# Optimization experiments

Hardware: AMD Instinct MI355X
Metric: run time of the kernel (lower is better)

The kernel has to match this reference:

```python
import jax, jax.numpy as jnp
import numpy as np

N = 100000   # nodes
E = 640000   # edges
D = 128      # init_node == hidden_node
L = 3        # layers (len('gcn_gcn_gcn'.split('_')))


def setup_inputs() -> dict:
    key = jax.random.key(0)
    ks = jax.random.split(key, 17)
    p = lambda k, shape: jax.random.normal(k, shape, jnp.float32) * 0.05
    return {
        "x": jax.random.normal(ks[0], (N, D), jnp.float32),
        "edge_attr": jax.random.uniform(ks[1], (E,), jnp.float32),
        "edge_index": jax.random.randint(ks[2], (2, E), 0, N),
        "conv_w": p(ks[3], (L, D, D)),       # SparseConv.weight
        "conv_lin_w": p(ks[4], (L, D, D)),   # SparseConv.lin (no bias)
        "l1_w": p(ks[5], (L, D, D)), "l1_b": p(ks[6], (L, D)),
        "l2_w": p(ks[7], (L, D, D)), "l2_b": p(ks[8], (L, D)),
        "mlp1_w": p(ks[9], (L, 2 * D, D)), "mlp1_b": p(ks[10], (L, D)),
        "mlp2_w": p(ks[11], (L, D, D)), "mlp2_b": p(ks[12], (L, D)),
        "post1_w": p(ks[13], (D, D)), "post1_b": p(ks[14], (D,)),
        "post2_w": p(ks[15], (D, D)), "post2_b": p(ks[16], (D,)),
    }


def reference(x, edge_attr, edge_index, conv_w, conv_lin_w,
              l1_w, l1_b, l2_w, l2_b, mlp1_w, mlp1_b, mlp2_w, mlp2_b,
              post1_w, post1_b, post2_w, post2_b):
    src, dst = edge_index[0], edge_index[1]  # PyG: message h_j from src, scatter-add at dst
    n = x.shape[0]

    def agg(h):
        # gather source features, weight per edge, scatter-add at targets
        return jax.ops.segment_sum(edge_attr[:, None] * h[src], dst, num_segments=n)

    mask = None
    for i in range(L):
        # --- WeightConv: computes sigmoid gate ---
        xm = x if mask is None else x * mask
        h = xm @ l1_w[i] + l1_b[i]
        w = jnp.concatenate([agg(h), xm @ l2_w[i] + l2_b[i]], axis=-1)  # [N, 2D]
        w = jax.nn.relu(jax.nn.relu(w) @ mlp1_w[i] + mlp1_b[i])
        mask = jax.nn.sigmoid(w @ mlp2_w[i] + mlp2_b[i])  # [N, D]
        # --- SparseConv: masked transform + propagate + residual lin ---
        h2 = (x * mask) @ conv_w[i]
        x = jax.nn.relu((agg(h2) + x @ conv_lin_w[i]) * mask)
    x = jax.nn.relu(x @ post1_w + post1_b)
    # F.dropout omitted (deterministic reference)
    return x @ post2_w + post2_b
```

## Files before the change

### kernel.cpp

```cpp
#include <hip/hip_runtime.h>
#include <math.h>

#define NN 100000
#define EE 640000
#define DD 128
#define NB_SCAN ((NN + 255) / 256)

typedef __attribute__((ext_vector_type(8))) short bf16x8;
typedef __attribute__((ext_vector_type(4))) float f32x4;

static __device__ __forceinline__ float4 ld4(const float* p) {
    return *reinterpret_cast<const float4*>(p);
}

static __device__ __forceinline__ unsigned short f2bf(float x) {
    unsigned u = __float_as_uint(x);
    return (unsigned short)((u + 0x7FFFu + ((u >> 16) & 1u)) >> 16);
}

static __device__ __forceinline__ void splitbf(float a, short& hi, short& lo) {
    unsigned u = __float_as_uint(a);
    unsigned hr = (u + 0x7FFFu + ((u >> 16) & 1u)) >> 16;
    float hf = __uint_as_float(hr << 16);
    float l = a - hf;
    unsigned ul = __float_as_uint(l);
    unsigned lr = (ul + 0x7FFFu + ((ul >> 16) & 1u)) >> 16;
    hi = (short)hr; lo = (short)lr;
}

__global__ void wfrag_k(const float* __restrict__ l1w, const float* __restrict__ l2w,
                        const float* __restrict__ mlp1w, const float* __restrict__ mlp2w,
                        const float* __restrict__ convw, const float* __restrict__ convlinw,
                        const float* __restrict__ post1w, const float* __restrict__ post2w,
                        unsigned short* __restrict__ Wh, unsigned short* __restrict__ Wl)
{
    const int b = blockIdx.x;
    const float* W; int slice; size_t fbase; int K;
    if (b < 12)      { W = l1w;      slice = b;      fbase = 0;      K = 128; }
    else if (b < 24) { W = l2w;      slice = b - 12; fbase = 49152;  K = 128; }
    else if (b < 48) { W = mlp1w;    slice = b - 24; fbase = 98304;  K = 256; }
    else if (b < 60) { W = mlp2w;    slice = b - 48; fbase = 196608; K = 128; }
    else if (b < 72) { W = convw;    slice = b - 60; fbase = 245760; K = 128; }
    else if (b < 84) { W = convlinw; slice = b - 72; fbase = 294912; K = 128; }
    else if (b < 88) { W = post1w;   slice = b - 84; fbase = 344064; K = 128; }
    else             { W = post2w;   slice = b - 88; fbase = 360448; K = 128; }
    const int kslices = K / 32;
    const int mat = slice / kslices;
    const int ks  = slice % kslices;
    const float* Wm = W + (size_t)mat * K * DD;
    const size_t outb = fbase + (size_t)mat * K * DD + (size_t)ks * 4096;
    const int t = threadIdx.x;
#pragma unroll
    for (int e = 0; e < 16; ++e) {
        const int f = t * 16 + e;
        const int r = f & 7, lane = (f >> 3) & 63, ct = f >> 9;
        const int krow = ks * 32 + (lane >> 4) * 8 + r;
        const int col  = ct * 16 + (lane & 15);
        short hh, ll;
        splitbf(Wm[(size_t)krow * DD + col], hh, ll);
        Wh[outb + f] = (unsigned short)hh; Wl[outb + f] = (unsigned short)ll;
    }
}

template<int KT, int DUAL, int RAW1, int MINW>
__launch_bounds__(256, MINW)
__global__ void gemm_f32A(const float* __restrict__ A,
                          const float* __restrict__ Amask,
                          const unsigned short* __restrict__ Wh0,
                          const unsigned short* __restrict__ Wl0,
                          const float* __restrict__ bias0, const int act0, const int obf0,
                          void* __restrict__ out0, const int ldo0, const int co0,
                          const unsigned short* __restrict__ Wh1,
                          const unsigned short* __restrict__ Wl1,
                          const float* __restrict__ bias1, const int obf1,
                          void* __restrict__ out1, const int ldo1, const int co1)
{
    __shared__ __align__(16) unsigned short Bs[16384];
    const int t = threadIdx.x, lane = t & 63, w = t >> 6;
    const int kg = lane >> 4, c16 = lane & 15;
    const int rb = blockIdx.x * 64 + w * 16;
    int ra = rb + c16; if (ra >= NN) ra = NN - 1;

    bf16x8 ah[KT], al[KT];
    bf16x8 uh[RAW1 ? KT : 1], ul[RAW1 ? KT : 1];
#pragma unroll
    for (int ks = 0; ks < KT; ++ks) {
        const float* ap = A + (size_t)ra * (KT * 32) + ks * 32 + kg * 8;
        const float4 v0 = ld4(ap), v1 = ld4(ap + 4);
        float tmp[8] = {v0.x, v0.y, v0.z, v0.w, v1.x, v1.y, v1.z, v1.w};
        if (RAW1) {
#pragma unroll
            for (int j = 0; j < 8; ++j) { short hh, ll; splitbf(tmp[j], hh, ll); uh[ks][j] = hh; ul[ks][j] = ll; }
        }
        if (Amask) {
            const float* mp = Amask + (size_t)ra * DD + ks * 32 + kg * 8;
            const float4 m0 = ld4(mp), m1 = ld4(mp + 4);
            tmp[0] *= m0.x; tmp[1] *= m0.y; tmp[2] *= m0.z; tmp[3] *= m0.w;
            tmp[4] *= m1.x; tmp[5] *= m1.y; tmp[6] *= m1.z; tmp[7] *= m1.w;
        }
#pragma unroll
        for (int j = 0; j < 8; ++j) { short hh, ll; splitbf(tmp[j], hh, ll); ah[ks][j] = hh; al[ks][j] = ll; }
    }

    auto pass = [&](const unsigned short* Wh, const unsigned short* Wl,
                    const bf16x8* xh, const bf16x8* xl,
                    const float* bias, const int act, const int obf,
                    void* out, const int ldo, const int co, const bool first) {
        f32x4 acc[8];
#pragma unroll
        for (int ct = 0; ct < 8; ++ct) acc[ct] = f32x4{0.f, 0.f, 0.f, 0.f};
#pragma unroll
        for (int st = 0; st < KT / 2; ++st) {
            if (!(first && st == 0)) __syncthreads();
#pragma unroll
            for (int i = 0; i < 4; ++i) {
                const int idx = i * 2048 + t * 8;
                *(uint4*)&Bs[idx]        = *(const uint4*)&Wh[(size_t)st * 8192 + idx];
                *(uint4*)&Bs[8192 + idx] = *(const uint4*)&Wl[(size_t)st * 8192 + idx];
            }
            __syncthreads();
#pragma unroll
            for (int s = 0; s < 2; ++s) {
                const int ks = st * 2 + s;
#pragma unroll
                for (int ct = 0; ct < 8; ++ct) {
                    const int fo = ((s * 8 + ct) * 64 + lane) * 8;
                    const bf16x8 bh = *(const bf16x8*)&Bs[fo];
                    const bf16x8 bl = *(const bf16x8*)&Bs[8192 + fo];
                    acc[ct] = __builtin_amdgcn_mfma_f32_16x16x32_bf16(xh[ks], bh, acc[ct], 0, 0, 0);
                    acc[ct] = __builtin_amdgcn_mfma_f32_16x16x32_bf16(xl[ks], bh, acc[ct], 0, 0, 0);
                    acc[ct] = __builtin_amdgcn_mfma_f32_16x16x32_bf16(xh[ks], bl, acc[ct], 0, 0, 0);
                }
            }
        }
#pragma unroll
        for (int ct = 0; ct < 8; ++ct) {
            const int c = ct * 16 + c16;
            const float b = bias ? bias[c] : 0.f;
#pragma unroll
            for (int r = 0; r < 4; ++r) {
                const int row = rb + kg * 4 + r;
                if (row < NN) {
                    float v = acc[ct][r] + b;
                    if (act == 1) v = fmaxf(v, 0.f);
                    if (obf) ((unsigned short*)out)[(size_t)row * ldo + co + c] = f2bf(v);
                    else     ((float*)out)[(size_t)row * ldo + co + c] = v;
                }
            }
        }
    };

    pass(Wh0, Wl0, ah, al, bias0, act0, obf0, out0, ldo0, co0, true);
    if (DUAL)
        pass(Wh1, Wl1, RAW1 ? uh : ah, RAW1 ? ul : al, bias1, 0, obf1, out1, ldo1, co1, false);
}

template<int KT, int MINW>
__launch_bounds__(256, MINW)
__global__ void gemm_bf16A(const unsigned short* __restrict__ A, const int reluA,
                           const unsigned short* __restrict__ Wh,
                           const unsigned short* __restrict__ Wl,
                           const float* __restrict__ bias, const int act, const int obf,
                           void* __restrict__ out, const int ldo, const int co)
{
    __shared__ __align__(16) unsigned short Bs[16384];
    const int t = threadIdx.x, lane = t & 63, w = t >> 6;
    const int kg = lane >> 4, c16 = lane & 15;
    const int rb = blockIdx.x * 64 + w * 16;
    int ra = rb + c16; if (ra >= NN) ra = NN - 1;

    bf16x8 ah[KT];
#pragma unroll
    for (int ks = 0; ks < KT; ++ks) {
        bf16x8 av = *(const bf16x8*)(A + (size_t)ra * (KT * 32) + ks * 32 + kg * 8);
        if (reluA) {
#pragma unroll
            for (int j = 0; j < 8; ++j) av[j] = (av[j] < 0) ? (short)0 : av[j];
        }
        ah[ks] = av;
    }

    f32x4 acc[8];
#pragma unroll
    for (int ct = 0; ct < 8; ++ct) acc[ct] = f32x4{0.f, 0.f, 0.f, 0.f};
#pragma unroll
    for (int st = 0; st < KT / 2; ++st) {
        if (st) __syncthreads();
#pragma unroll
        for (int i = 0; i < 4; ++i) {
            const int idx = i * 2048 + t * 8;
            *(uint4*)&Bs[idx]        = *(const uint4*)&Wh[(size_t)st * 8192 + idx];
            *(uint4*)&Bs[8192 + idx] = *(const uint4*)&Wl[(size_t)st * 8192 + idx];
        }
        __syncthreads();
#pragma unroll
        for (int s = 0; s < 2; ++s) {
            const int ks = st * 2 + s;
#pragma unroll
            for (int ct = 0; ct < 8; ++ct) {
                const int fo = ((s * 8 + ct) * 64 + lane) * 8;
                const bf16x8 bh = *(const bf16x8*)&Bs[fo];
                const bf16x8 bl = *(const bf16x8*)&Bs[8192 + fo];
                acc[ct] = __builtin_amdgcn_mfma_f32_16x16x32_bf16(ah[ks], bh, acc[ct], 0, 0, 0);
                acc[ct] = __builtin_amdgcn_mfma_f32_16x16x32_bf16(ah[ks], bl, acc[ct], 0, 0, 0);
            }
        }
    }
#pragma unroll
    for (int ct = 0; ct < 8; ++ct) {
        const int c = ct * 16 + c16;
        const float b = bias ? bias[c] : 0.f;
#pragma unroll
        for (int r = 0; r < 4; ++r) {
            const int row = rb + kg * 4 + r;
            if (row < NN) {
                float v = acc[ct][r] + b;
                if (act == 1) v = fmaxf(v, 0.f);
                else if (act == 2) v = 1.f / (1.f + __expf(-v));
                if (obf) ((unsigned short*)out)[(size_t)row * ldo + co + c] = f2bf(v);
                else     ((float*)out)[(size_t)row * ldo + co + c] = v;
            }
        }
    }
}

__launch_bounds__(256)
__global__ void spmm_bf16(const unsigned int* __restrict__ H2,
                          const int* __restrict__ rp,
                          const int* __restrict__ ccol,
                          const float* __restrict__ cval,
                          const float* __restrict__ addend,
                          const float* __restrict__ pmask,
                          const int act, const int obf,
                          float* __restrict__ outf, unsigned int* __restrict__ outb,
                          const int ldo)
{
    const int w = (blockIdx.x * 256 + threadIdx.x) >> 6;
    if (w >= NN) return;
    const int lane = threadIdx.x & 63;
    const int s = rp[w], e = rp[w + 1];
    float ax = 0.f, ay = 0.f;
    int j = s;
    while (j < e) {
        int cnt = e - j; if (cnt > 8) cnt = 8;
        int cols[8]; float vals[8];
#pragma unroll
        for (int q = 0; q < 8; ++q) {
            if (q < cnt) { cols[q] = ccol[j + q]; vals[q] = cval[j + q]; }
        }
#pragma unroll
        for (int q = 0; q < 8; ++q) {
            if (q < cnt) {
                const unsigned u = H2[(size_t)cols[q] * 64 + lane];
                ax = fmaf(vals[q], __uint_as_float(u << 16), ax);
                ay = fmaf(vals[q], __uint_as_float(u & 0xFFFF0000u), ay);
            }
        }
        j += cnt;
    }
    if (addend) {
        const float2 t = *reinterpret_cast<const float2*>(addend + (size_t)w * DD + lane * 2);
        ax += t.x; ay += t.y;
    }
    if (pmask) {
        const float2 m = *reinterpret_cast<const float2*>(pmask + (size_t)w * DD + lane * 2);
        ax *= m.x; ay *= m.y;
    }
    if (act == 1) { ax = fmaxf(ax, 0.f); ay = fmaxf(ay, 0.f); }
    if (obf) {
        outb[(size_t)w * ldo + lane] = (unsigned)f2bf(ax) | ((unsigned)f2bf(ay) << 16);
    } else {
        float2 o; o.x = ax; o.y = ay;
        *reinterpret_cast<float2*>(outf + (size_t)w * ldo + lane * 2) = o;
    }
}

__global__ void hist_k(const int* __restrict__ dstI, int* __restrict__ counts) {
    const int e = blockIdx.x * 256 + threadIdx.x;
    if (e < EE) atomicAdd(&counts[dstI[e]], 1);
}

__global__ void block_sums_k(const int* __restrict__ counts, int* __restrict__ bsum) {
    __shared__ int s[256];
    const int t = threadIdx.x;
    const int i = blockIdx.x * 256 + t;
    s[t] = (i < NN) ? counts[i] : 0;
    __syncthreads();
    for (int off = 128; off > 0; off >>= 1) {
        if (t < off) s[t] += s[t + off];
        __syncthreads();
    }
    if (t == 0) bsum[blockIdx.x] = s[0];
}

__global__ void scan_bsums_k(const int* __restrict__ bsum, int* __restrict__ bpre, const int nb) {
    __shared__ int s[512];
    const int t = threadIdx.x;
    s[t] = (t < nb) ? bsum[t] : 0;
    __syncthreads();
    for (int off = 1; off < 512; off <<= 1) {
        const int tmp = (t >= off) ? s[t - off] : 0;
        __syncthreads();
        s[t] += tmp;
        __syncthreads();
    }
    if (t < nb) bpre[t] = (t == 0) ? 0 : s[t - 1];
}

__global__ void scan_final_k(const int* __restrict__ counts, const int* __restrict__ bpre,
                             int* __restrict__ rowptr, int* __restrict__ nextc) {
    __shared__ int s[256];
    const int t = threadIdx.x;
    const int i = blockIdx.x * 256 + t;
    const int v = (i < NN) ? counts[i] : 0;
    s[t] = v;
    __syncthreads();
    for (int off = 1; off < 256; off <<= 1) {
        const int tmp = (t >= off) ? s[t - off] : 0;
        __syncthreads();
        s[t] += tmp;
        __syncthreads();
    }
    const int excl = s[t] - v + bpre[blockIdx.x];
    if (i < NN) { rowptr[i] = excl; nextc[i] = excl; }
    if (i == NN - 1) rowptr[NN] = EE;
}

__global__ void scatter_k(const int* __restrict__ srcI, const int* __restrict__ dstI,
                          const float* __restrict__ ea, int* __restrict__ nextc,
                          int* __restrict__ ccol, float* __restrict__ cval) {
    const int e = blockIdx.x * 256 + threadIdx.x;
    if (e >= EE) return;
    const int d = dstI[e];
    const int p = atomicAdd(&nextc[d], 1);
    ccol[p] = srcI[e];
    cval[p] = ea[e];
}

extern "C" void kernel_launch(void* const* d_in, const int* in_sizes, int n_in,
                              void* d_out, int out_size, void* d_ws, size_t ws_size,
                              hipStream_t stream)
{
    const float* x_in0      = (const float*)d_in[0];
    const float* edge_attr  = (const float*)d_in[1];
    const int*   edge_index = (const int*)d_in[2];
    const float* l1_b       = (const float*)d_in[6];
    const float* l2_b       = (const float*)d_in[8];
    const float* mlp1_b     = (const float*)d_in[10];
    const float* mlp2_b     = (const float*)d_in[12];
    const float* post1_b    = (const float*)d_in[14];
    const float* post2_b    = (const float*)d_in[16];

    const int* srcI = edge_index;
    const int* dstI = edge_index + EE;

    float* x_ws = (float*)d_out;

    float*          maskb  = (float*)d_ws;
    float*          tbuf   = maskb + (size_t)NN * DD;
    unsigned short* h16    = (unsigned short*)(tbuf + (size_t)NN * DD);
    unsigned short* cat16  = h16 + (size_t)NN * DD;
    unsigned short* gh16   = cat16 + (size_t)NN * 2 * DD;
    unsigned short* Wh_all = gh16 + (size_t)NN * DD;
    unsigned short* Wl_all = Wh_all + 376832;
    float* cval   = (float*)(Wl_all + 376832);
    int*   ccol   = (int*)(cval + EE);
    int*   rowptr = ccol + EE;
    int*   nextc  = rowptr + (NN + 1);
    int*   counts = nextc + NN;
    int*   bsum   = counts + NN;
    int*   bpre   = bsum + 512;

    wfrag_k<<<92, 256, 0, stream>>>((const float*)d_in[5], (const float*)d_in[7],
                                    (const float*)d_in[9], (const float*)d_in[11],
                                    (const float*)d_in[3], (const float*)d_in[4],
                                    (const float*)d_in[13], (const float*)d_in[15],
                                    Wh_all, Wl_all);
    hipMemsetAsync(counts, 0, NN * sizeof(int), stream);
    hist_k      <<<(EE + 255) / 256, 256, 0, stream>>>(dstI, counts);
    block_sums_k<<<NB_SCAN, 256, 0, stream>>>(counts, bsum);
    scan_bsums_k<<<1, 512, 0, stream>>>(bsum, bpre, NB_SCAN);
    scan_final_k<<<NB_SCAN, 256, 0, stream>>>(counts, bpre, rowptr, nextc);
    scatter_k   <<<(EE + 255) / 256, 256, 0, stream>>>(srcI, dstI, edge_attr, nextc, ccol, cval);

    const int GG = (NN + 63) / 64;
    const int SPMM_GRID = NN * 64 / 256;

    const size_t F_L1 = 0, F_L2 = 49152, F_M1 = 98304, F_M2 = 196608;
    const size_t F_CV = 245760, F_CL = 294912, F_P1 = 344064, F_P2 = 360448;

    for (int i = 0; i < 3; ++i) {
        const float* xc = (i == 0) ? x_in0 : x_ws;
        const float* pm = (i == 0) ? nullptr : maskb;
        const size_t o128 = (size_t)i * 16384, o256 = (size_t)i * 32768;
        gemm_f32A<4, 1, 0, 4><<<GG, 256, 0, stream>>>(xc, pm,
            Wh_all + F_L1 + o128, Wl_all + F_L1 + o128, l1_b + (size_t)i * DD, 0, 1, h16, DD, 0,
            Wh_all + F_L2 + o128, Wl_all + F_L2 + o128, l2_b + (size_t)i * DD, 1, cat16, 2 * DD, DD);
        spmm_bf16<<<SPMM_GRID, 256, 0, stream>>>((const unsigned*)h16, rowptr, ccol, cval,
            nullptr, nullptr, 0, 1, nullptr, (unsigned*)cat16, 2 * DD / 2);
        gemm_bf16A<8, 4><<<GG, 256, 0, stream>>>(cat16, 1,
            Wh_all + F_M1 + o256, Wl_all + F_M1 + o256, mlp1_b + (size_t)i * DD, 1, 1, gh16, DD, 0);
        gemm_bf16A<4, 4><<<GG, 256, 0, stream>>>(gh16, 0,
            Wh_all + F_M2 + o128, Wl_all + F_M2 + o128, mlp2_b + (size_t)i * DD, 2, 0, maskb, DD, 0);
        gemm_f32A<4, 1, 1, 3><<<GG, 256, 0, stream>>>(xc, maskb,
            Wh_all + F_CV + o128, Wl_all + F_CV + o128, nullptr, 0, 1, h16, DD, 0,
            Wh_all + F_CL + o128, Wl_all + F_CL + o128, nullptr, 0, tbuf, DD, 0);
        spmm_bf16<<<SPMM_GRID, 256, 0, stream>>>((const unsigned*)h16, rowptr, ccol, cval,
            tbuf, maskb, 1, 0, x_ws, nullptr, DD);
    }
    gemm_f32A<4, 0, 0, 4><<<GG, 256, 0, stream>>>(x_ws, nullptr,
        Wh_all + F_P1, Wl_all + F_P1, post1_b, 1, 1, gh16, DD, 0,
        nullptr, nullptr, nullptr, 0, nullptr, 0, 0);
    gemm_bf16A<4, 4><<<GG, 256, 0, stream>>>(gh16, 0,
        Wh_all + F_P2, Wl_all + F_P2, post2_b, 0, 0, (float*)d_out, DD, 0);

    (void)in_sizes; (void)n_in; (void)out_size; (void)ws_size;
}
```

Before: 1.187 ms.

## Fuse MLP GEMM pairs, store x as bf16 hi/lo splits, vectorize epilogues

```diff
diff --git a/kernel.cpp b/kernel.cpp
--- a/kernel.cpp
+++ b/kernel.cpp
@@ -5,34 +5,46 @@
 #define EE 640000
 #define DD 128
 #define NB_SCAN ((NN + 255) / 256)
+#define GG 1563
 
 typedef __attribute__((ext_vector_type(8))) short bf16x8;
 typedef __attribute__((ext_vector_type(4))) float f32x4;
+typedef unsigned short ush;
+typedef unsigned int uint;
 
 static __device__ __forceinline__ float4 ld4(const float* p) {
     return *reinterpret_cast<const float4*>(p);
 }
-
-static __device__ __forceinline__ unsigned short f2bf(float x) {
+static __device__ __forceinline__ ush f2bf(float x) {
     unsigned u = __float_as_uint(x);
-    return (unsigned short)((u + 0x7FFFu + ((u >> 16) & 1u)) >> 16);
-}
-
+    return (ush)((u + 0x7FFFu + ((u >> 16) & 1u)) >> 16);
+}
+static __device__ __forceinline__ float bf2f(short h) {
+    return __uint_as_float(((unsigned)(ush)h) << 16);
+}
 static __device__ __forceinline__ void splitbf(float a, short& hi, short& lo) {
     unsigned u = __float_as_uint(a);
     unsigned hr = (u + 0x7FFFu + ((u >> 16) & 1u)) >> 16;
-    float hf = __uint_as_float(hr << 16);
-    float l = a - hf;
+    float l = a - __uint_as_float(hr << 16);
     unsigned ul = __float_as_uint(l);
-    unsigned lr = (ul + 0x7FFFu + ((ul >> 16) & 1u)) >> 16;
-    hi = (short)hr; lo = (short)lr;
+    hi = (short)hr; lo = (short)((ul + 0x7FFFu + ((ul >> 16) & 1u)) >> 16);
+}
+static __device__ __forceinline__ void splitbf_t(float a, short& hi, short& lo) {
+    unsigned u = __float_as_uint(a);
+    hi = (short)(u >> 16);
+    float l = a - __uint_as_float(u & 0xFFFF0000u);
+    lo = (short)(__float_as_uint(l) >> 16);
+}
+
+static __device__ __forceinline__ f32x4 MFMA(bf16x8 a, bf16x8 b, f32x4 c) {
+    return __builtin_amdgcn_mfma_f32_16x16x32_bf16(a, b, c, 0, 0, 0);
 }
 
 __global__ void wfrag_k(const float* __restrict__ l1w, const float* __restrict__ l2w,
                         const float* __restrict__ mlp1w, const float* __restrict__ mlp2w,
                         const float* __restrict__ convw, const float* __restrict__ convlinw,
                         const float* __restrict__ post1w, const float* __restrict__ post2w,
-                        unsigned short* __restrict__ Wh, unsigned short* __restrict__ Wl)
+                        ush* __restrict__ Wh, ush* __restrict__ Wl)
 {
     const int b = blockIdx.x;
     const float* W; int slice; size_t fbase; int K;
@@ -55,142 +67,238 @@
         const int f = t * 16 + e;
         const int r = f & 7, lane = (f >> 3) & 63, ct = f >> 9;
         const int krow = ks * 32 + (lane >> 4) * 8 + r;
-        const int col  = ct * 16 + (lane & 15);
+        const int col  = (lane & 15) * 8 + ct;
         short hh, ll;
         splitbf(Wm[(size_t)krow * DD + col], hh, ll);
-        Wh[outb + f] = (unsigned short)hh; Wl[outb + f] = (unsigned short)ll;
-    }
-}
-
-template<int KT, int DUAL, int RAW1, int MINW>
+        Wh[outb + f] = (ush)hh; Wl[outb + f] = (ush)ll;
+    }
+}
+
+template<bool THREE>
+static __device__ __forceinline__ void mfma_pass128(
+    const bf16x8* xh, const bf16x8* xl,
+    const ush* __restrict__ Wh, const ush* __restrict__ Wl,
+    ush* Bs, const int t, const int lane, const bool first, f32x4* acc)
+{
+#pragma unroll
+    for (int ct = 0; ct < 8; ++ct) acc[ct] = f32x4{0.f, 0.f, 0.f, 0.f};
+#pragma unroll
+    for (int st = 0; st < 2; ++st) {
+        if (!(first && st == 0)) __syncthreads();
+#pragma unroll
+        for (int i = 0; i < 4; ++i) {
+            const int idx = i * 2048 + t * 8;
+            *(uint4*)&Bs[idx]        = *(const uint4*)&Wh[(size_t)st * 8192 + idx];
+            *(uint4*)&Bs[8192 + idx] = *(const uint4*)&Wl[(size_t)st * 8192 + idx];
+        }
+        __syncthreads();
+#pragma unroll
+        for (int s = 0; s < 2; ++s) {
+            const int ks = st * 2 + s;
+#pragma unroll
+            for (int ct = 0; ct < 8; ++ct) {
+                const int fo = ((s * 8 + ct) * 64 + lane) * 8;
+                const bf16x8 bh = *(const bf16x8*)&Bs[fo];
+                const bf16x8 bl = *(const bf16x8*)&Bs[8192 + fo];
+                acc[ct] = MFMA(xh[ks], bh, acc[ct]);
+                if (THREE) acc[ct] = MFMA(xl[ks], bh, acc[ct]);
+                acc[ct] = MFMA(xh[ks], bl, acc[ct]);
+            }
+        }
+    }
+}
+
+static __device__ __forceinline__ void epi_store(
+    const f32x4* acc, const float* __restrict__ bias, const int act, const int obf,
+    void* __restrict__ out, const int ldo, const int co,
+    const int rb, const int kg, const int c16)
+{
+    float bv[8];
+    if (bias) {
+        const float4 b0 = ld4(bias + c16 * 8), b1 = ld4(bias + c16 * 8 + 4);
+        bv[0]=b0.x; bv[1]=b0.y; bv[2]=b0.z; bv[3]=b0.w;
+        bv[4]=b1.x; bv[5]=b1.y; bv[6]=b1.z; bv[7]=b1.w;
+    } else {
+#pragma unroll
+        for (int j = 0; j < 8; ++j) bv[j] = 0.f;
+    }
+#pragma unroll
+    for (int r = 0; r < 4; ++r) {
+        const int row = rb + kg * 4 + r;
+        if (row < NN) {
+            float v[8];
+#pragma unroll
+            for (int ct = 0; ct < 8; ++ct) {
+                v[ct] = acc[ct][r] + bv[ct];
+                if (act == 1) v[ct] = fmaxf(v[ct], 0.f);
+                else if (act == 2) v[ct] = 1.f / (1.f + __expf(-v[ct]));
+            }
+            if (obf) {
+                uint4 pk;
+                pk.x = (uint)f2bf(v[0]) | ((uint)f2bf(v[1]) << 16);
+                pk.y = (uint)f2bf(v[2]) | ((uint)f2bf(v[3]) << 16);
+                pk.z = (uint)f2bf(v[4]) | ((uint)f2bf(v[5]) << 16);
+                pk.w = (uint)f2bf(v[6]) | ((uint)f2bf(v[7]) << 16);
+                *(uint4*)((ush*)out + (size_t)row * ldo + co + c16 * 8) = pk;
+            } else {
+                float* op = (float*)out + (size_t)row * ldo + co + c16 * 8;
+                *(float4*)op       = make_float4(v[0], v[1], v[2], v[3]);
+                *(float4*)(op + 4) = make_float4(v[4], v[5], v[6], v[7]);
+            }
+        }
+    }
+}
+
+template<int RAW1, int MINW>
 __launch_bounds__(256, MINW)
 __global__ void gemm_f32A(const float* __restrict__ A,
                           const float* __restrict__ Amask,
-                          const unsigned short* __restrict__ Wh0,
-                          const unsigned short* __restrict__ Wl0,
+                          const ush* __restrict__ Wh0, const ush* __restrict__ Wl0,
                           const float* __restrict__ bias0, const int act0, const int obf0,
                           void* __restrict__ out0, const int ldo0, const int co0,
-                          const unsigned short* __restrict__ Wh1,
-                          const unsigned short* __restrict__ Wl1,
-                          const float* __restrict__ bias1, const int obf1,
+                          const ush* __restrict__ Wh1, const ush* __restrict__ Wl1,
+                          const float* __restrict__ bias1, const int act1, const int obf1,
                           void* __restrict__ out1, const int ldo1, const int co1)
 {
-    __shared__ __align__(16) unsigned short Bs[16384];
+    __shared__ __align__(16) ush Bs[16384];
     const int t = threadIdx.x, lane = t & 63, w = t >> 6;
     const int kg = lane >> 4, c16 = lane & 15;
     const int rb = blockIdx.x * 64 + w * 16;
     int ra = rb + c16; if (ra >= NN) ra = NN - 1;
 
-    bf16x8 ah[KT], al[KT];
-    bf16x8 uh[RAW1 ? KT : 1], ul[RAW1 ? KT : 1];
-#pragma unroll
-    for (int ks = 0; ks < KT; ++ks) {
-        const float* ap = A + (size_t)ra * (KT * 32) + ks * 32 + kg * 8;
+    bf16x8 ah[4], al[4];
+    bf16x8 uh[RAW1 ? 4 : 1], ul[RAW1 ? 4 : 1];
+#pragma unroll
+    for (int ks = 0; ks < 4; ++ks) {
+        const float* ap = A + (size_t)ra * DD + ks * 32 + kg * 8;
         const float4 v0 = ld4(ap), v1 = ld4(ap + 4);
         float tmp[8] = {v0.x, v0.y, v0.z, v0.w, v1.x, v1.y, v1.z, v1.w};
         if (RAW1) {
 #pragma unroll
-            for (int j = 0; j < 8; ++j) { short hh, ll; splitbf(tmp[j], hh, ll); uh[ks][j] = hh; ul[ks][j] = ll; }
+            for (int j = 0; j < 8; ++j) { short hh, ll; splitbf_t(tmp[j], hh, ll); uh[ks][j] = hh; ul[ks][j] = ll; }
         }
         if (Amask) {
             const float* mp = Amask + (size_t)ra * DD + ks * 32 + kg * 8;
             const float4 m0 = ld4(mp), m1 = ld4(mp + 4);
-            tmp[0] *= m0.x; tmp[1] *= m0.y; tmp[2] *= m0.z; tmp[3] *= m0.w;
-            tmp[4] *= m1.x; tmp[5] *= m1.y; tmp[6] *= m1.z; tmp[7] *= m1.w;
-        }
-#pragma unroll
-        for (int j = 0; j < 8; ++j) { short hh, ll; splitbf(tmp[j], hh, ll); ah[ks][j] = hh; al[ks][j] = ll; }
-    }
-
-    auto pass = [&](const unsigned short* Wh, const unsigned short* Wl,
-                    const bf16x8* xh, const bf16x8* xl,
-                    const float* bias, const int act, const int obf,
-                    void* out, const int ldo, const int co, const bool first) {
-        f32x4 acc[8];
-#pragma unroll
-        for (int ct = 0; ct < 8; ++ct) acc[ct] = f32x4{0.f, 0.f, 0.f, 0.f};
-#pragma unroll
-        for (int st = 0; st < KT / 2; ++st) {
-            if (!(first && st == 0)) __syncthreads();
-#pragma unroll
-            for (int i = 0; i < 4; ++i) {
-                const int idx = i * 2048 + t * 8;
-                *(uint4*)&Bs[idx]        = *(const uint4*)&Wh[(size_t)st * 8192 + idx];
-                *(uint4*)&Bs[8192 + idx] = *(const uint4*)&Wl[(size_t)st * 8192 + idx];
-            }
-            __syncthreads();
-#pragma unroll
-            for (int s = 0; s < 2; ++s) {
-                const int ks = st * 2 + s;
-#pragma unroll
-                for (int ct = 0; ct < 8; ++ct) {
-                    const int fo = ((s * 8 + ct) * 64 + lane) * 8;
-                    const bf16x8 bh = *(const bf16x8*)&Bs[fo];
-                    const bf16x8 bl = *(const bf16x8*)&Bs[8192 + fo];
-                    acc[ct] = __builtin_amdgcn_mfma_f32_16x16x32_bf16(xh[ks], bh, acc[ct], 0, 0, 0);
-                    acc[ct] = __builtin_amdgcn_mfma_f32_16x16x32_bf16(xl[ks], bh, acc[ct], 0, 0, 0);
-                    acc[ct] = __builtin_amdgcn_mfma_f32_16x16x32_bf16(xh[ks], bl, acc[ct], 0, 0, 0);
-                }
-            }
-        }
-#pragma unroll
-        for (int ct = 0; ct < 8; ++ct) {
-            const int c = ct * 16 + c16;
-            const float b = bias ? bias[c] : 0.f;
-#pragma unroll
-            for (int r = 0; r < 4; ++r) {
-                const int row = rb + kg * 4 + r;
-                if (row < NN) {
-                    float v = acc[ct][r] + b;
-                    if (act == 1) v = fmaxf(v, 0.f);
-                    if (obf) ((unsigned short*)out)[(size_t)row * ldo + co + c] = f2bf(v);
-                    else     ((float*)out)[(size_t)row * ldo + co + c] = v;
-                }
-            }
-        }
-    };
-
-    pass(Wh0, Wl0, ah, al, bias0, act0, obf0, out0, ldo0, co0, true);
-    if (DUAL)
-        pass(Wh1, Wl1, RAW1 ? uh : ah, RAW1 ? ul : al, bias1, 0, obf1, out1, ldo1, co1, false);
-}
-
-template<int KT, int MINW>
-__launch_bounds__(256, MINW)
-__global__ void gemm_bf16A(const unsigned short* __restrict__ A, const int reluA,
-                           const unsigned short* __restrict__ Wh,
-                           const unsigned short* __restrict__ Wl,
-                           const float* __restrict__ bias, const int act, const int obf,
-                           void* __restrict__ out, const int ldo, const int co)
-{
-    __shared__ __align__(16) unsigned short Bs[16384];
+            tmp[0]*=m0.x; tmp[1]*=m0.y; tmp[2]*=m0.z; tmp[3]*=m0.w;
+            tmp[4]*=m1.x; tmp[5]*=m1.y; tmp[6]*=m1.z; tmp[7]*=m1.w;
+        }
+#pragma unroll
+        for (int j = 0; j < 8; ++j) { short hh, ll; splitbf_t(tmp[j], hh, ll); ah[ks][j] = hh; al[ks][j] = ll; }
+    }
+
+    f32x4 acc[8];
+    mfma_pass128<true>(ah, al, Wh0, Wl0, Bs, t, lane, true, acc);
+    epi_store(acc, bias0, act0, obf0, out0, ldo0, co0, rb, kg, c16);
+    mfma_pass128<true>(RAW1 ? uh : ah, RAW1 ? ul : al, Wh1, Wl1, Bs, t, lane, false, acc);
+    epi_store(acc, bias1, act1, obf1, out1, ldo1, co1, rb, kg, c16);
+}
+
+__launch_bounds__(256, 4)
+__global__ void gemm_xm(const ush* __restrict__ Ah, const ush* __restrict__ Al,
+                        const ush* __restrict__ Wh0, const ush* __restrict__ Wl0,
+                        const float* __restrict__ bias0, void* __restrict__ out0,
+                        const int ldo0, const int co0,
+                        const ush* __restrict__ Wh1, const ush* __restrict__ Wl1,
+                        const float* __restrict__ bias1, void* __restrict__ out1,
+                        const int ldo1, const int co1)
+{
+    __shared__ __align__(16) ush Bs[16384];
     const int t = threadIdx.x, lane = t & 63, w = t >> 6;
     const int kg = lane >> 4, c16 = lane & 15;
     const int rb = blockIdx.x * 64 + w * 16;
     int ra = rb + c16; if (ra >= NN) ra = NN - 1;
 
-    bf16x8 ah[KT];
-#pragma unroll
-    for (int ks = 0; ks < KT; ++ks) {
-        bf16x8 av = *(const bf16x8*)(A + (size_t)ra * (KT * 32) + ks * 32 + kg * 8);
+    bf16x8 amh[4], aml[4];
+#pragma unroll
+    for (int ks = 0; ks < 4; ++ks) {
+        amh[ks] = *(const bf16x8*)(Ah + (size_t)ra * DD + ks * 32 + kg * 8);
+        aml[ks] = *(const bf16x8*)(Al + (size_t)ra * DD + ks * 32 + kg * 8);
+    }
+    f32x4 acc[8];
+    mfma_pass128<true>(amh, aml, Wh0, Wl0, Bs, t, lane, true, acc);
+    epi_store(acc, bias0, 0, 1, out0, ldo0, co0, rb, kg, c16);
+    mfma_pass128<true>(amh, aml, Wh1, Wl1, Bs, t, lane, false, acc);
+    epi_store(acc, bias1, 0, 1, out1, ldo1, co1, rb, kg, c16);
+}
+
+__launch_bounds__(256, 3)
+__global__ void gemm_conv(const ush* __restrict__ Ah, const ush* __restrict__ Al,
+                          const float* __restrict__ mask,
+                          const ush* __restrict__ WhC, const ush* __restrict__ WlC,
+                          void* __restrict__ outH,
+                          const ush* __restrict__ WhL, const ush* __restrict__ WlL,
+                          void* __restrict__ outT)
+{
+    __shared__ __align__(16) ush Bs[16384];
+    const int t = threadIdx.x, lane = t & 63, w = t >> 6;
+    const int kg = lane >> 4, c16 = lane & 15;
+    const int rb = blockIdx.x * 64 + w * 16;
+    int ra = rb + c16; if (ra >= NN) ra = NN - 1;
+
+    bf16x8 uh[4], ul[4], amh[4], aml[4];
+#pragma unroll
+    for (int ks = 0; ks < 4; ++ks) {
+        uh[ks] = *(const bf16x8*)(Ah + (size_t)ra * DD + ks * 32 + kg * 8);
+        ul[ks] = *(const bf16x8*)(Al + (size_t)ra * DD + ks * 32 + kg * 8);
+        const float* mp = mask + (size_t)ra * DD + ks * 32 + kg * 8;
+        const float4 m0 = ld4(mp), m1 = ld4(mp + 4);
+        const float mv[8] = {m0.x, m0.y, m0.z, m0.w, m1.x, m1.y, m1.z, m1.w};
+#pragma unroll
+        for (int j = 0; j < 8; ++j) {
+            const float af = bf2f(uh[ks][j]) + bf2f(ul[ks][j]);
+            short hh, ll; splitbf_t(af * mv[j], hh, ll);
+            amh[ks][j] = hh; aml[ks][j] = ll;
+        }
+    }
+    f32x4 acc[8];
+    mfma_pass128<true>(amh, aml, WhC, WlC, Bs, t, lane, true, acc);
+    epi_store(acc, nullptr, 0, 1, outH, DD, 0, rb, kg, c16);
+    mfma_pass128<true>(uh, ul, WhL, WlL, Bs, t, lane, false, acc);
+    epi_store(acc, nullptr, 0, 1, outT, DD, 0, rb, kg, c16);
+}
+
+template<int KT1, int AHL, int SIGE>
+__launch_bounds__(256, 3)
+__global__ void gemm_fused2(const ush* __restrict__ Aa, const ush* __restrict__ Ab,
+                            const int reluA,
+                            const ush* __restrict__ W1h, const ush* __restrict__ W1l,
+                            const float* __restrict__ b1,
+                            const ush* __restrict__ W2h, const ush* __restrict__ W2l,
+                            const float* __restrict__ b2,
+                            float* __restrict__ out)
+{
+    __shared__ __align__(16) ush Bs[16384];
+    __shared__ __align__(16) ush Ts[8192];
+    const int t = threadIdx.x, lane = t & 63, w = t >> 6;
+    const int kg = lane >> 4, c16 = lane & 15;
+    const int rb = blockIdx.x * 64 + w * 16;
+    int ra = rb + c16; if (ra >= NN) ra = NN - 1;
+    char* tsb = (char*)&Ts[w * 2048];
+
+    bf16x8 a1h[KT1], a1l[AHL ? KT1 : 1];
+#pragma unroll
+    for (int ks = 0; ks < KT1; ++ks) {
+        bf16x8 av = *(const bf16x8*)(Aa + (size_t)ra * (KT1 * 32) + ks * 32 + kg * 8);
         if (reluA) {
 #pragma unroll
             for (int j = 0; j < 8; ++j) av[j] = (av[j] < 0) ? (short)0 : av[j];
         }
-        ah[ks] = av;
+        a1h[ks] = av;
+        if (AHL) a1l[ks] = *(const bf16x8*)(Ab + (size_t)ra * (KT1 * 32) + ks * 32 + kg * 8);
     }
 
     f32x4 acc[8];
 #pragma unroll
     for (int ct = 0; ct < 8; ++ct) acc[ct] = f32x4{0.f, 0.f, 0.f, 0.f};
 #pragma unroll
-    for (int st = 0; st < KT / 2; ++st) {
+    for (int st = 0; st < KT1 / 2; ++st) {
         if (st) __syncthreads();
 #pragma unroll
         for (int i = 0; i < 4; ++i) {
             const int idx = i * 2048 + t * 8;
-            *(uint4*)&Bs[idx]        = *(const uint4*)&Wh[(size_t)st * 8192 + idx];
-            *(uint4*)&Bs[8192 + idx] = *(const uint4*)&Wl[(size_t)st * 8192 + idx];
+            *(uint4*)&Bs[idx]        = *(const uint4*)&W1h[(size_t)st * 8192 + idx];
+            *(uint4*)&Bs[8192 + idx] = *(const uint4*)&W1l[(size_t)st * 8192 + idx];
         }
         __syncthreads();
 #pragma unroll
@@ -201,39 +309,73 @@
                 const int fo = ((s * 8 + ct) * 64 + lane) * 8;
                 const bf16x8 bh = *(const bf16x8*)&Bs[fo];
                 const bf16x8 bl = *(const bf16x8*)&Bs[8192 + fo];
-                acc[ct] = __builtin_amdgcn_mfma_f32_16x16x32_bf16(ah[ks], bh, acc[ct], 0, 0, 0);
-                acc[ct] = __builtin_amdgcn_mfma_f32_16x16x32_bf16(ah[ks], bl, acc[ct], 0, 0, 0);
+                acc[ct] = MFMA(a1h[ks], bh, acc[ct]);
+                if (AHL) acc[ct] = MFMA(a1l[ks], bh, acc[ct]);
+                acc[ct] = MFMA(a1h[ks], bl, acc[ct]);
             }
         }
     }
-#pragma unroll
-    for (int ct = 0; ct < 8; ++ct) {
-        const int c = ct * 16 + c16;
-        const float b = bias ? bias[c] : 0.f;
+
+    {
+        const float4 b0 = ld4(b1 + c16 * 8), b1v = ld4(b1 + c16 * 8 + 4);
+        const float bv[8] = {b0.x, b0.y, b0.z, b0.w, b1v.x, b1v.y, b1v.z, b1v.w};
 #pragma unroll
         for (int r = 0; r < 4; ++r) {
-            const int row = rb + kg * 4 + r;
-            if (row < NN) {
-                float v = acc[ct][r] + b;
-                if (act == 1) v = fmaxf(v, 0.f);
-                else if (act == 2) v = 1.f / (1.f + __expf(-v));
-                if (obf) ((unsigned short*)out)[(size_t)row * ldo + co + c] = f2bf(v);
-                else     ((float*)out)[(size_t)row * ldo + co + c] = v;
+            const int row = kg * 4 + r;
+            bf16x8 pk;
+#pragma unroll
+            for (int ct = 0; ct < 8; ++ct)
+                pk[ct] = (short)f2bf(fmaxf(acc[ct][r] + bv[ct], 0.f));
+            const int byte = (row * 256 + c16 * 16) ^ ((row & 7) << 4);
+            *(bf16x8*)(tsb + byte) = pk;
+        }
+    }
+    bf16x8 a2[4];
+#pragma unroll
+    for (int ks2 = 0; ks2 < 4; ++ks2) {
+        const int byte = (c16 * 256 + ks2 * 64 + kg * 16) ^ ((c16 & 7) << 4);
+        a2[ks2] = *(const bf16x8*)(tsb + byte);
+    }
+
+#pragma unroll
+    for (int ct = 0; ct < 8; ++ct) acc[ct] = f32x4{0.f, 0.f, 0.f, 0.f};
+#pragma unroll
+    for (int st = 0; st < 2; ++st) {
+        __syncthreads();
+#pragma unroll
+        for (int i = 0; i < 4; ++i) {
+            const int idx = i * 2048 + t * 8;
+            *(uint4*)&Bs[idx]        = *(const uint4*)&W2h[(size_t)st * 8192 + idx];
+            *(uint4*)&Bs[8192 + idx] = *(const uint4*)&W2l[(size_t)st * 8192 + idx];
+        }
+        __syncthreads();
+#pragma unroll
+        for (int s = 0; s < 2; ++s) {
+            const int ks = st * 2 + s;
+#pragma unroll
+            for (int ct = 0; ct < 8; ++ct) {
+                const int fo = ((s * 8 + ct) * 64 + lane) * 8;
+                const bf16x8 bh = *(const bf16x8*)&Bs[fo];
+                const bf16x8 bl = *(const bf16x8*)&Bs[8192 + fo];
+                acc[ct] = MFMA(a2[ks], bh, acc[ct]);
+                acc[ct] = MFMA(a2[ks], bl, acc[ct]);
             }
         }
     }
-}
-
+    epi_store(acc, b2, SIGE ? 2 : 0, 0, out, DD, 0, rb, kg, c16);
+}
+
+template<int XOUT>
 __launch_bounds__(256)
-__global__ void spmm_bf16(const unsigned int* __restrict__ H2,
-                          const int* __restrict__ rp,
-                          const int* __restrict__ ccol,
-                          const float* __restrict__ cval,
-                          const float* __restrict__ addend,
-                          const float* __restrict__ pmask,
-                          const int act, const int obf,
-                          float* __restrict__ outf, unsigned int* __restrict__ outb,
-                          const int ldo)
+__global__ void spmm_b(const uint* __restrict__ H2,
+                       const int* __restrict__ rp,
+                       const int* __restrict__ ccol,
+                       const float* __restrict__ cval,
+                       const uint* __restrict__ tadd,
+                       const float* __restrict__ pmask,
+                       uint* __restrict__ o0, uint* __restrict__ o1,
+                       uint* __restrict__ o2, uint* __restrict__ o3,
+                       const int ldo, const int writeXM)
 {
     const int w = (blockIdx.x * 256 + threadIdx.x) >> 6;
     if (w >= NN) return;
@@ -245,33 +387,38 @@
         int cnt = e - j; if (cnt > 8) cnt = 8;
         int cols[8]; float vals[8];
 #pragma unroll
-        for (int q = 0; q < 8; ++q) {
+        for (int q = 0; q < 8; ++q)
             if (q < cnt) { cols[q] = ccol[j + q]; vals[q] = cval[j + q]; }
-        }
 #pragma unroll
         for (int q = 0; q < 8; ++q) {
             if (q < cnt) {
-                const unsigned u = H2[(size_t)cols[q] * 64 + lane];
+                const uint u = H2[(size_t)cols[q] * 64 + lane];
                 ax = fmaf(vals[q], __uint_as_float(u << 16), ax);
                 ay = fmaf(vals[q], __uint_as_float(u & 0xFFFF0000u), ay);
             }
         }
         j += cnt;
     }
-    if (addend) {
-        const float2 t = *reinterpret_cast<const float2*>(addend + (size_t)w * DD + lane * 2);
-        ax += t.x; ay += t.y;
-    }
-    if (pmask) {
+    if (XOUT == 0) {
+        o0[(size_t)w * ldo + lane] = (uint)f2bf(ax) | ((uint)f2bf(ay) << 16);
+    } else {
+        const uint tu = tadd[(size_t)w * 64 + lane];
+        ax += __uint_as_float(tu << 16);
+        ay += __uint_as_float(tu & 0xFFFF0000u);
         const float2 m = *reinterpret_cast<const float2*>(pmask + (size_t)w * DD + lane * 2);
-        ax *= m.x; ay *= m.y;
-    }
-    if (act == 1) { ax = fmaxf(ax, 0.f); ay = fmaxf(ay, 0.f); }
-    if (obf) {
-        outb[(size_t)w * ldo + lane] = (unsigned)f2bf(ax) | ((unsigned)f2bf(ay) << 16);
-    } else {
-        float2 o; o.x = ax; o.y = ay;
-        *reinterpret_cast<float2*>(outf + (size_t)w * ldo + lane * 2) = o;
+        ax = fmaxf(ax * m.x, 0.f);
+        ay = fmaxf(ay * m.y, 0.f);
+        short xh0, xl0, xh1, xl1;
+        splitbf_t(ax, xh0, xl0); splitbf_t(ay, xh1, xl1);
+        o0[(size_t)w * 64 + lane] = (uint)(ush)xh0 | ((uint)(ush)xh1 << 16);
+        o1[(size_t)w * 64 + lane] = (uint)(ush)xl0 | ((uint)(ush)xl1 << 16);
+        if (writeXM) {
+            const float mx = ax * m.x, my = ay * m.y;
+            short mh0, ml0, mh1, ml1;
+            splitbf_t(mx, mh0, ml0); splitbf_t(my, mh1, ml1);
+            o2[(size_t)w * 64 + lane] = (uint)(ush)mh0 | ((uint)(ush)mh1 << 16);
+            o3[(size_t)w * 64 + lane] = (uint)(ush)ml0 | ((uint)(ush)ml1 << 16);
+        }
     }
 }
 
@@ -279,7 +426,6 @@
     const int e = blockIdx.x * 256 + threadIdx.x;
     if (e < EE) atomicAdd(&counts[dstI[e]], 1);
 }
-
 __global__ void block_sums_k(const int* __restrict__ counts, int* __restrict__ bsum) {
     __shared__ int s[256];
     const int t = threadIdx.x;
@@ -292,7 +438,6 @@
     }
     if (t == 0) bsum[blockIdx.x] = s[0];
 }
-
 __global__ void scan_bsums_k(const int* __restrict__ bsum, int* __restrict__ bpre, const int nb) {
     __shared__ int s[512];
     const int t = threadIdx.x;
@@ -306,7 +451,6 @@
     }
     if (t < nb) bpre[t] = (t == 0) ? 0 : s[t - 1];
 }
-
 __global__ void scan_final_k(const int* __restrict__ counts, const int* __restrict__ bpre,
                              int* __restrict__ rowptr, int* __restrict__ nextc) {
     __shared__ int s[256];
@@ -325,7 +469,6 @@
     if (i < NN) { rowptr[i] = excl; nextc[i] = excl; }
     if (i == NN - 1) rowptr[NN] = EE;
 }
-
 __global__ void scatter_k(const int* __restrict__ srcI, const int* __restrict__ dstI,
                           const float* __restrict__ ea, int* __restrict__ nextc,
                           int* __restrict__ ccol, float* __restrict__ cval) {
@@ -354,22 +497,24 @@
     const int* srcI = edge_index;
     const int* dstI = edge_index + EE;
 
-    float* x_ws = (float*)d_out;
-
-    float*          maskb  = (float*)d_ws;
-    float*          tbuf   = maskb + (size_t)NN * DD;
-    unsigned short* h16    = (unsigned short*)(tbuf + (size_t)NN * DD);
-    unsigned short* cat16  = h16 + (size_t)NN * DD;
-    unsigned short* gh16   = cat16 + (size_t)NN * 2 * DD;
-    unsigned short* Wh_all = gh16 + (size_t)NN * DD;
-    unsigned short* Wl_all = Wh_all + 376832;
-    float* cval   = (float*)(Wl_all + 376832);
-    int*   ccol   = (int*)(cval + EE);
-    int*   rowptr = ccol + EE;
-    int*   nextc  = rowptr + (NN + 1);
-    int*   counts = nextc + NN;
-    int*   bsum   = counts + NN;
-    int*   bpre   = bsum + 512;
+    float* maskb = (float*)d_out;
+
+    ush* xh     = (ush*)d_ws;
+    ush* xl     = xh  + (size_t)NN * DD;
+    ush* xmh    = xl  + (size_t)NN * DD;
+    ush* xml    = xmh + (size_t)NN * DD;
+    ush* h16    = xml + (size_t)NN * DD;
+    ush* cat16  = h16 + (size_t)NN * DD;
+    ush* t16    = cat16;
+    ush* Wh_all = cat16 + (size_t)NN * 2 * DD;
+    ush* Wl_all = Wh_all + 376832;
+    float* cval = (float*)(Wl_all + 376832);
+    int* ccol   = (int*)(cval + EE);
+    int* rowptr = ccol + EE;
+    int* nextc  = rowptr + (NN + 1);
+    int* counts = nextc + NN;
+    int* bsum   = counts + NN;
+    int* bpre   = bsum + 512;
 
     wfrag_k<<<92, 256, 0, stream>>>((const float*)d_in[5], (const float*)d_in[7],
                                     (const float*)d_in[9], (const float*)d_in[11],
@@ -383,36 +528,41 @@
     scan_final_k<<<NB_SCAN, 256, 0, stream>>>(counts, bpre, rowptr, nextc);
     scatter_k   <<<(EE + 255) / 256, 256, 0, stream>>>(srcI, dstI, edge_attr, nextc, ccol, cval);
 
-    const int GG = (NN + 63) / 64;
     const int SPMM_GRID = NN * 64 / 256;
-
     const size_t F_L1 = 0, F_L2 = 49152, F_M1 = 98304, F_M2 = 196608;
     const size_t F_CV = 245760, F_CL = 294912, F_P1 = 344064, F_P2 = 360448;
 
     for (int i = 0; i < 3; ++i) {
-        const float* xc = (i == 0) ? x_in0 : x_ws;
-        const float* pm = (i == 0) ? nullptr : maskb;
         const size_t o128 = (size_t)i * 16384, o256 = (size_t)i * 32768;
-        gemm_f32A<4, 1, 0, 4><<<GG, 256, 0, stream>>>(xc, pm,
-            Wh_all + F_L1 + o128, Wl_all + F_L1 + o128, l1_b + (size_t)i * DD, 0, 1, h16, DD, 0,
-            Wh_all + F_L2 + o128, Wl_all + F_L2 + o128, l2_b + (size_t)i * DD, 1, cat16, 2 * DD, DD);
-        spmm_bf16<<<SPMM_GRID, 256, 0, stream>>>((const unsigned*)h16, rowptr, ccol, cval,
-            nullptr, nullptr, 0, 1, nullptr, (unsigned*)cat16, 2 * DD / 2);
-        gemm_bf16A<8, 4><<<GG, 256, 0, stream>>>(cat16, 1,
-            Wh_all + F_M1 + o256, Wl_all + F_M1 + o256, mlp1_b + (size_t)i * DD, 1, 1, gh16, DD, 0);
-        gemm_bf16A<4, 4><<<GG, 256, 0, stream>>>(gh16, 0,
-            Wh_all + F_M2 + o128, Wl_all + F_M2 + o128, mlp2_b + (size_t)i * DD, 2, 0, maskb, DD, 0);
-        gemm_f32A<4, 1, 1, 3><<<GG, 256, 0, stream>>>(xc, maskb,
-            Wh_all + F_CV + o128, Wl_all + F_CV + o128, nullptr, 0, 1, h16, DD, 0,
-            Wh_all + F_CL + o128, Wl_all + F_CL + o128, nullptr, 0, tbuf, DD, 0);
-        spmm_bf16<<<SPMM_GRID, 256, 0, stream>>>((const unsigned*)h16, rowptr, ccol, cval,
-            tbuf, maskb, 1, 0, x_ws, nullptr, DD);
-    }
-    gemm_f32A<4, 0, 0, 4><<<GG, 256, 0, stream>>>(x_ws, nullptr,
-        Wh_all + F_P1, Wl_all + F_P1, post1_b, 1, 1, gh16, DD, 0,
-        nullptr, nullptr, nullptr, 0, nullptr, 0, 0);
-    gemm_bf16A<4, 4><<<GG, 256, 0, stream>>>(gh16, 0,
-        Wh_all + F_P2, Wl_all + F_P2, post2_b, 0, 0, (float*)d_out, DD, 0);
+        if (i == 0) {
+            gemm_f32A<0, 4><<<GG, 256, 0, stream>>>(x_in0, nullptr,
+                Wh_all + F_L1, Wl_all + F_L1, l1_b, 0, 1, h16, DD, 0,
+                Wh_all + F_L2, Wl_all + F_L2, l2_b, 0, 1, cat16, 2 * DD, DD);
+        } else {
+            gemm_xm<<<GG, 256, 0, stream>>>(xmh, xml,
+                Wh_all + F_L1 + o128, Wl_all + F_L1 + o128, l1_b + (size_t)i * DD, h16, DD, 0,
+                Wh_all + F_L2 + o128, Wl_all + F_L2 + o128, l2_b + (size_t)i * DD, cat16, 2 * DD, DD);
+        }
+        spmm_b<0><<<SPMM_GRID, 256, 0, stream>>>((const uint*)h16, rowptr, ccol, cval,
+            nullptr, nullptr, (uint*)cat16, nullptr, nullptr, nullptr, 128, 0);
+        gemm_fused2<8, 0, 1><<<GG, 256, 0, stream>>>(cat16, nullptr, 1,
+            Wh_all + F_M1 + o256, Wl_all + F_M1 + o256, mlp1_b + (size_t)i * DD,
+            Wh_all + F_M2 + o128, Wl_all + F_M2 + o128, mlp2_b + (size_t)i * DD, maskb);
+        if (i == 0) {
+            gemm_f32A<1, 3><<<GG, 256, 0, stream>>>(x_in0, maskb,
+                Wh_all + F_CV, Wl_all + F_CV, nullptr, 0, 1, h16, DD, 0,
+                Wh_all + F_CL, Wl_all + F_CL, nullptr, 0, 1, t16, DD, 0);
+        } else {
+            gemm_conv<<<GG, 256, 0, stream>>>(xh, xl, maskb,
+                Wh_all + F_CV + o128, Wl_all + F_CV + o128, h16,
+                Wh_all + F_CL + o128, Wl_all + F_CL + o128, t16);
+        }
+        spmm_b<1><<<SPMM_GRID, 256, 0, stream>>>((const uint*)h16, rowptr, ccol, cval,
+            (const uint*)t16, maskb, (uint*)xh, (uint*)xl, (uint*)xmh, (uint*)xml, 64, (i < 2) ? 1 : 0);
+    }
+    gemm_fused2<4, 1, 0><<<GG, 256, 0, stream>>>(xh, xl, 0,
+        Wh_all + F_P1, Wl_all + F_P1, post1_b,
+        Wh_all + F_P2, Wl_all + F_P2, post2_b, (float*)d_out);
 
     (void)in_sizes; (void)n_in; (void)out_size; (void)ws_size;
 }
```

Measured after the change: 953.3 us. -19.7%, faster.
